# Performance work log

Measured on AMD Instinct MI355X. Metric: run time of the kernel, lower is better.

## Reference

```python
import jax, jax.numpy as jnp
import numpy as np

N = 5          # ngram order
N_SYM = 64     # alphabet size
D = N_SYM * (N - 1)
B, L = 32, 4096


def setup_inputs() -> dict:
    key = jax.random.key(0)
    kx, kw, kb = jax.random.split(key, 3)
    x = jax.random.randint(kx, (B, L), 0, N_SYM, dtype=jnp.int64)
    # nn.Linear(D, N_sym): W is (N_sym, D), b is (N_sym,)
    bound = 1.0 / np.sqrt(D)
    W = jax.random.uniform(kw, (N_SYM, D), jnp.float32, -bound, bound)
    b = jax.random.uniform(kb, (N_SYM,), jnp.float32, -bound, bound)
    return {"x": x, "W": W, "b": b}


def _encode(x):
    # ngram at output position j covers x[:, j-n+1 : j] (length n-1, excludes j)
    # windows: (B, L-(n-1), n-1)
    win = jnp.stack([x[:, p : L - (N - 1) + p] for p in range(N - 1)], axis=-1)
    oh = jax.nn.one_hot(win, N_SYM, dtype=jnp.float32)  # (B, L', n-1, N_sym)
    # torch flattens enc[(sym, pos)] row-major -> feature = sym*(n-1)+pos
    oh = jnp.transpose(oh, (0, 1, 3, 2)).reshape(B, L - (N - 1), D)
    # positions j < n-1 are all-zero rows
    return jnp.pad(oh, ((0, 0), (N - 1, 0), (0, 0)))  # (B, L, D)


def reference(x, W, b):
    enc = _encode(x)                                   # (B, L, D)
    logits = jnp.einsum('bld,vd->blv', enc, W) + b     # (B, L, N_sym)
    return logits
```

## Files before the change

### kernel.cpp

```cpp
#include <hip/hip_runtime.h>


#define NSYM   64
#define CTX    4
#define DFEAT  256
#define LSEQ   4096
#define BATCH  32
#define NPOS   (BATCH * LSEQ)
#define NITER  (NPOS / 4)
#define ITERS_PER_WAVE 16
#define BLOCKS (NITER / (ITERS_PER_WAVE * 4))

__global__ __launch_bounds__(256, 2)
void loglinear_kernel(const int* __restrict__ x,
                      const float* __restrict__ W,
                      const float* __restrict__ bias,
                      float* __restrict__ out) {
    __shared__ float wt[DFEAT * NSYM];

    const int t = threadIdx.x;

    {
        const int v = t & 63;
        const int chunk = t >> 6;
        #pragma unroll
        for (int it = 0; it < 16; ++it) {
            const int f4 = chunk * 16 + it;
            const int d0 = f4 * 4;
            const float4 w = *reinterpret_cast<const float4*>(W + v * DFEAT + d0);
            const float wv[4] = {w.x, w.y, w.z, w.w};
            #pragma unroll
            for (int k = 0; k < 4; ++k) {
                const int d = d0 + k;
                const int addr = d * 64 + ((((v >> 2) ^ (d & 15)) << 2) | (v & 3));
                wt[addr] = wv[k];
            }
        }
    }
    __syncthreads();

    const int lane = t & 63;
    const int wave = t >> 6;
    const int g = lane >> 4;
    const int q = lane & 15;

    const float4 b4 = reinterpret_cast<const float4*>(bias)[q];

    const int gw = blockIdx.x * 4 + wave;
    const int i0 = gw * ITERS_PER_WAVE;
    float4* __restrict__ out4 = reinterpret_cast<float4*>(out);

    #pragma unroll 4
    for (int ii = 0; ii < ITERS_PER_WAVE; ++ii) {
        const int i = i0 + ii;
        const int P = i * 4 + g;
        const int bi = P >> 12;
        const int j = P & (LSEQ - 1);
        float4 acc = b4;
        if (j >= CTX) {
            const int* xp = x + bi * LSEQ + j - CTX;
            #pragma unroll
            for (int p = 0; p < CTX; ++p) {
                const int c = xp[p] * 4 + p;
                const float4 w = *reinterpret_cast<const float4*>(
                    wt + c * 64 + ((q ^ (c & 15)) << 2));
                acc.x += w.x; acc.y += w.y; acc.z += w.z; acc.w += w.w;
            }
        }
        out4[(size_t)P * 16 + q] = acc;
    }
}

extern "C" void kernel_launch(void* const* d_in, const int* in_sizes, int n_in,
                              void* d_out, int out_size, void* d_ws, size_t ws_size,
                              hipStream_t stream) {
    const int*   x  = (const int*)d_in[0];
    const float* W  = (const float*)d_in[1];
    const float* b  = (const float*)d_in[2];
    float*       out = (float*)d_out;

    hipLaunchKernelGGL(loglinear_kernel, dim3(BLOCKS), dim3(256), 0, stream,
                       x, W, b, out);
}
```

Baseline: 17.12 us.

## Store weight table in LDS as bf16 pairs, shrink per-wave work, nontemporal stores

The transposed weight table in shared memory is now packed as bf16 pairs, halving LDS from 64KB to 32KB. That allows four blocks per CU under the new launch bounds and halves the per-lookup LDS read width. Iterations per wave drop from 16 to 8, doubling the block count, and output stores become nontemporal. Rounding the weights to bf16 adds numerical error to the logits, which may exceed tolerance.

```diff
diff --git a/kernel.cpp b/kernel.cpp
--- a/kernel.cpp
+++ b/kernel.cpp
@@ -7,33 +7,42 @@
 #define LSEQ   4096
 #define BATCH  32
 #define NPOS   (BATCH * LSEQ)
-#define NITER  (NPOS / 4)
-#define ITERS_PER_WAVE 16
-#define BLOCKS (NITER / (ITERS_PER_WAVE * 4))
+#define IPW    8
+#define WAVES  4
+#define POS_PER_BLOCK (WAVES * 4 * IPW)
+#define BLOCKS (NPOS / POS_PER_BLOCK)
 
-__global__ __launch_bounds__(256, 2)
+typedef float vfloat4 __attribute__((ext_vector_type(4)));
+
+static __device__ __forceinline__ unsigned f2bf(float f) {
+    unsigned u = __float_as_uint(f);
+    return (u + 0x7fffu + ((u >> 16) & 1u)) >> 16;
+}
+
+__global__ __launch_bounds__(256, 4)
 void loglinear_kernel(const int* __restrict__ x,
                       const float* __restrict__ W,
                       const float* __restrict__ bias,
                       float* __restrict__ out) {
-    __shared__ float wt[DFEAT * NSYM];
+    __shared__ unsigned int wt[DFEAT * 32];
 
     const int t = threadIdx.x;
 
     {
-        const int v = t & 63;
-        const int chunk = t >> 6;
+        const int vp    = t & 31;
+        const int chunk = t >> 5;
+        const int q = vp >> 1, h = vp & 1;
         #pragma unroll
-        for (int it = 0; it < 16; ++it) {
-            const int f4 = chunk * 16 + it;
-            const int d0 = f4 * 4;
-            const float4 w = *reinterpret_cast<const float4*>(W + v * DFEAT + d0);
-            const float wv[4] = {w.x, w.y, w.z, w.w};
+        for (int it = 0; it < 8; ++it) {
+            const int d0 = (chunk * 8 + it) * 4;
+            const float4 a = *reinterpret_cast<const float4*>(W + (2*vp)     * DFEAT + d0);
+            const float4 b = *reinterpret_cast<const float4*>(W + (2*vp + 1) * DFEAT + d0);
+            const float av[4] = {a.x, a.y, a.z, a.w};
+            const float bv[4] = {b.x, b.y, b.z, b.w};
             #pragma unroll
             for (int k = 0; k < 4; ++k) {
                 const int d = d0 + k;
-                const int addr = d * 64 + ((((v >> 2) ^ (d & 15)) << 2) | (v & 3));
-                wt[addr] = wv[k];
+                wt[d*32 + (((q ^ (d & 15)) << 1) + h)] = f2bf(av[k]) | (f2bf(bv[k]) << 16);
             }
         }
     }
@@ -44,39 +53,42 @@
     const int g = lane >> 4;
     const int q = lane & 15;
 
-    const float4 b4 = reinterpret_cast<const float4*>(bias)[q];
+    const float4 bq = reinterpret_cast<const float4*>(bias)[q];
+    const vfloat4 b4 = {bq.x, bq.y, bq.z, bq.w};
 
-    const int gw = blockIdx.x * 4 + wave;
-    const int i0 = gw * ITERS_PER_WAVE;
-    float4* __restrict__ out4 = reinterpret_cast<float4*>(out);
+    const int gw = blockIdx.x * WAVES + wave;
+    const int i0 = gw * IPW;
+    vfloat4* __restrict__ out4 = reinterpret_cast<vfloat4*>(out);
 
-    #pragma unroll 4
-    for (int ii = 0; ii < ITERS_PER_WAVE; ++ii) {
-        const int i = i0 + ii;
-        const int P = i * 4 + g;
+    #pragma unroll
+    for (int ii = 0; ii < IPW; ++ii) {
+        const int P  = (i0 + ii) * 4 + g;
         const int bi = P >> 12;
-        const int j = P & (LSEQ - 1);
-        float4 acc = b4;
+        const int j  = P & (LSEQ - 1);
+        vfloat4 acc = b4;
         if (j >= CTX) {
             const int* xp = x + bi * LSEQ + j - CTX;
             #pragma unroll
             for (int p = 0; p < CTX; ++p) {
                 const int c = xp[p] * 4 + p;
-                const float4 w = *reinterpret_cast<const float4*>(
-                    wt + c * 64 + ((q ^ (c & 15)) << 2));
-                acc.x += w.x; acc.y += w.y; acc.z += w.z; acc.w += w.w;
+                const uint2 wp = *reinterpret_cast<const uint2*>(
+                    &wt[c*32 + ((q ^ (c & 15)) << 1)]);
+                acc.x += __uint_as_float(wp.x << 16);
+                acc.y += __uint_as_float(wp.x & 0xffff0000u);
+                acc.z += __uint_as_float(wp.y << 16);
+                acc.w += __uint_as_float(wp.y & 0xffff0000u);
             }
         }
-        out4[(size_t)P * 16 + q] = acc;
+        __builtin_nontemporal_store(acc, &out4[(size_t)P * 16 + q]);
     }
 }
 
 extern "C" void kernel_launch(void* const* d_in, const int* in_sizes, int n_in,
                               void* d_out, int out_size, void* d_ws, size_t ws_size,
                               hipStream_t stream) {
-    const int*   x  = (const int*)d_in[0];
-    const float* W  = (const float*)d_in[1];
-    const float* b  = (const float*)d_in[2];
+    const int*   x   = (const int*)d_in[0];
+    const float* W   = (const float*)d_in[1];
+    const float* b   = (const float*)d_in[2];
     float*       out = (float*)d_out;
 
     hipLaunchKernelGGL(loglinear_kernel, dim3(BLOCKS), dim3(256), 0, stream,
```

Result: slower. 18.99 us (+11.0%).
